# Kernel tuning notes

Hardware: AMD Instinct MI355X
Metric: run time of the kernel (lower is better)

## Reference

```python
import jax, jax.numpy as jnp
import numpy as np

EPS = 1e-12  # F.normalize eps


def quat2matrix(J):
    # J: [B, N, D, 4] in (x, y, z, w) order; normalized then reordered to (w, x, y, z)
    norm = jnp.sqrt(jnp.sum(J * J, axis=-1, keepdims=True))
    Jn = J / jnp.maximum(norm, EPS)
    x, y, z, w = Jn[..., 0], Jn[..., 1], Jn[..., 2], Jn[..., 3]
    # pytorch3d quaternion_to_matrix with q = (r, i, j, k) = (w, x, y, z)
    two_s = 2.0 / (w * w + x * x + y * y + z * z)
    r00 = 1.0 - two_s * (y * y + z * z)
    r01 = two_s * (x * y - z * w)
    r02 = two_s * (x * z + y * w)
    r10 = two_s * (x * y + z * w)
    r11 = 1.0 - two_s * (x * x + z * z)
    r12 = two_s * (y * z - x * w)
    r20 = two_s * (x * z - y * w)
    r21 = two_s * (y * z + x * w)
    r22 = 1.0 - two_s * (x * x + y * y)
    R = jnp.stack([
        jnp.stack([r00, r01, r02], axis=-1),
        jnp.stack([r10, r11, r12], axis=-1),
        jnp.stack([r20, r21, r22], axis=-1),
    ], axis=-2)  # [B, N, D, 3, 3]
    return R


def setup_inputs() -> dict:
    key = jax.random.key(0)
    k1, k2, k3, k4, k5 = jax.random.split(key, 5)
    Bb, N, D, F = 8, 4096, 256, 256  # batch, points, in_channels, out_channels
    return {
        "X": jax.random.normal(k1, (Bb, N, D, 3), dtype=jnp.float32),
        "J": jax.random.normal(k2, (Bb, N, D, 4), dtype=jnp.float32),
        "A": jax.random.normal(k3, (F, D), dtype=jnp.float32),
        "B": jax.random.normal(k4, (F, D), dtype=jnp.float32),
        "C": jax.random.normal(k5, (F, D), dtype=jnp.float32),
    }


def reference(X, J, A, B, C):
    R = quat2matrix(J)  # [B, N, D, 3, 3]
    # RTX[..., i] = (R^T X)_i = sum_k R[..., k, i] * X[..., k]
    RTX = jnp.einsum('bndki,bndk->bndi', R, X)  # [B, N, D, 3]
    rt0 = RTX[..., 0:1]
    rt1 = RTX[..., 1:2]
    rt2 = RTX[..., 2:3]
    # get_rrtx(i, R, s) = R[..., :, i] * s (column i of R scaled by scalar)
    a_term = R[..., :, 0] * rt0 + R[..., :, 1] * rt1  # [B, N, D, 3]
    b_term = R[..., :, 1] * rt0 - R[..., :, 0] * rt1
    c_term = R[..., :, 2] * rt2
    Y = (jnp.einsum('fe,bnei->bnfi', A, a_term)
         + jnp.einsum('fe,bnei->bnfi', B, b_term)
         + jnp.einsum('fe,bnei->bnfi', C, c_term))  # [B, N, F, 3]
    return Y
```

## Files before the change

kernel.cpp:

```cpp
#include <hip/hip_runtime.h>


typedef __bf16 bf16_t;
typedef __attribute__((ext_vector_type(8))) __bf16 bf16x8;
typedef __attribute__((ext_vector_type(4))) __bf16 bf16x4;
typedef __attribute__((ext_vector_type(4))) float f32x4;

constexpr int Dd  = 256;
constexpr int Gp  = 16;
constexpr int TPB = 512;

__device__ __forceinline__ bf16_t to_bf16(float f) {
    unsigned u = __builtin_bit_cast(unsigned, f);
    u += 0x7FFFu + ((u >> 16) & 1u);
    unsigned short h = (unsigned short)(u >> 16);
    return __builtin_bit_cast(bf16_t, h);
}

__device__ __forceinline__ int swz(int row, int k) {
    return row * 768 + (k ^ ((row & 7) << 3));
}

__global__ __launch_bounds__(256)
void convert_w_kernel(const float* __restrict__ A, const float* __restrict__ B,
                      const float* __restrict__ C, bf16_t* __restrict__ W)
{
    const int e4 = (blockIdx.x * 256 + threadIdx.x) * 4;
    const float* src;
    if (e4 < 65536)        src = A + e4;
    else if (e4 < 131072)  src = B + (e4 - 65536);
    else                   src = C + (e4 - 131072);
    const float4 v = *reinterpret_cast<const float4*>(src);
    bf16x4 o;
    o[0] = to_bf16(v.x); o[1] = to_bf16(v.y); o[2] = to_bf16(v.z); o[3] = to_bf16(v.w);
    *reinterpret_cast<bf16x4*>(W + e4) = o;
}

__global__ __launch_bounds__(TPB, 4)
void alaq_mfma_kernel(const float* __restrict__ X, const float* __restrict__ J,
                      const bf16_t* __restrict__ W, float* __restrict__ Y)
{
    __shared__ bf16_t TT[48 * 768];

    const int tid = threadIdx.x;
    const long bn0 = (long)blockIdx.x * Gp;
    const long ebase = bn0 * Dd;

    float4 qv[8];
    float  xv[8][3];
    #pragma unroll
    for (int rr = 0; rr < 8; ++rr) {
        const long base = ebase + rr * TPB + tid;
        qv[rr] = *reinterpret_cast<const float4*>(J + base * 4);
        const float* xp = X + base * 3;
        xv[rr][0] = xp[0]; xv[rr][1] = xp[1]; xv[rr][2] = xp[2];
    }

    #pragma unroll
    for (int rr = 0; rr < 8; ++rr) {
        const int idx = rr * TPB + tid;
        const int p = idx >> 8;
        const int e = idx & 255;

        const float4 q = qv[rr];
        const float x0 = xv[rr][0], x1 = xv[rr][1], x2 = xv[rr][2];

        const float nsq = q.x*q.x + q.y*q.y + q.z*q.z + q.w*q.w;
        const float inv = 1.0f / fmaxf(sqrtf(nsq), 1e-12f);
        const float qx = q.x*inv, qy = q.y*inv, qz = q.z*inv, qw = q.w*inv;
        const float s = 2.0f / (qw*qw + qx*qx + qy*qy + qz*qz);

        const float r00 = 1.0f - s*(qy*qy + qz*qz);
        const float r01 = s*(qx*qy - qz*qw);
        const float r02 = s*(qx*qz + qy*qw);
        const float r10 = s*(qx*qy + qz*qw);
        const float r11 = 1.0f - s*(qx*qx + qz*qz);
        const float r12 = s*(qy*qz - qx*qw);
        const float r20 = s*(qx*qz - qy*qw);
        const float r21 = s*(qy*qz + qx*qw);
        const float r22 = 1.0f - s*(qx*qx + qy*qy);

        const float rt0 = r00*x0 + r10*x1 + r20*x2;
        const float rt1 = r01*x0 + r11*x1 + r21*x2;
        const float rt2 = r02*x0 + r12*x1 + r22*x2;

        const int row = p * 3;
        TT[swz(row    ,       e)] = to_bf16(r00*rt0 + r01*rt1);
        TT[swz(row + 1,       e)] = to_bf16(r10*rt0 + r11*rt1);
        TT[swz(row + 2,       e)] = to_bf16(r20*rt0 + r21*rt1);
        TT[swz(row    , 256 + e)] = to_bf16(r01*rt0 - r00*rt1);
        TT[swz(row + 1, 256 + e)] = to_bf16(r11*rt0 - r10*rt1);
        TT[swz(row + 2, 256 + e)] = to_bf16(r21*rt0 - r20*rt1);
        TT[swz(row    , 512 + e)] = to_bf16(r02*rt2);
        TT[swz(row + 1, 512 + e)] = to_bf16(r12*rt2);
        TT[swz(row + 2, 512 + e)] = to_bf16(r22*rt2);
    }
    __syncthreads();

    const int w  = tid >> 6;
    const int l  = tid & 63;
    const int lr = l & 15;
    const int lq = l >> 4;

    f32x4 acc[3][2] = {};

    const int f0 = (2 * w) * 16 + lr;
    const bf16_t* Wf0 = W + f0 * 256 + (lq << 3);
    const bf16_t* Wf1 = Wf0 + 16 * 256;
    const int swzmask = (lr & 7) << 3;

    #pragma unroll
    for (int k0 = 0; k0 < 24; ++k0) {
        const int term = k0 >> 3;
        const int eb   = (k0 & 7) << 5;
        const bf16x8 b0 = *reinterpret_cast<const bf16x8*>(Wf0 + (term << 16) + eb);
        const bf16x8 b1 = *reinterpret_cast<const bf16x8*>(Wf1 + (term << 16) + eb);

        const int kswz = (((k0 << 5) + (lq << 3)) ^ swzmask);
        const bf16x8 a0 = *reinterpret_cast<const bf16x8*>(&TT[         lr  * 768 + kswz]);
        const bf16x8 a1 = *reinterpret_cast<const bf16x8*>(&TT[(16 +    lr) * 768 + kswz]);
        const bf16x8 a2 = *reinterpret_cast<const bf16x8*>(&TT[(32 +    lr) * 768 + kswz]);

        acc[0][0] = __builtin_amdgcn_mfma_f32_16x16x32_bf16(a0, b0, acc[0][0], 0, 0, 0);
        acc[1][0] = __builtin_amdgcn_mfma_f32_16x16x32_bf16(a1, b0, acc[1][0], 0, 0, 0);
        acc[2][0] = __builtin_amdgcn_mfma_f32_16x16x32_bf16(a2, b0, acc[2][0], 0, 0, 0);
        acc[0][1] = __builtin_amdgcn_mfma_f32_16x16x32_bf16(a0, b1, acc[0][1], 0, 0, 0);
        acc[1][1] = __builtin_amdgcn_mfma_f32_16x16x32_bf16(a1, b1, acc[1][1], 0, 0, 0);
        acc[2][1] = __builtin_amdgcn_mfma_f32_16x16x32_bf16(a2, b1, acc[2][1], 0, 0, 0);
    }

    #pragma unroll
    for (int mi = 0; mi < 3; ++mi) {
        #pragma unroll
        for (int ni = 0; ni < 2; ++ni) {
            const int f = (2 * w + ni) * 16 + lr;
            #pragma unroll
            for (int r = 0; r < 4; ++r) {
                const int m = mi * 16 + lq * 4 + r;
                const int p = m / 3;
                const int i = m - p * 3;
                Y[(bn0 + p) * 768 + f * 3 + i] = acc[mi][ni][r];
            }
        }
    }
}

extern "C" void kernel_launch(void* const* d_in, const int* in_sizes, int n_in,
                              void* d_out, int out_size, void* d_ws, size_t ws_size,
                              hipStream_t stream) {
    const float* X  = (const float*)d_in[0];
    const float* J  = (const float*)d_in[1];
    const float* A  = (const float*)d_in[2];
    const float* B  = (const float*)d_in[3];
    const float* Cm = (const float*)d_in[4];
    float* Y = (float*)d_out;
    bf16_t* W = (bf16_t*)d_ws;

    convert_w_kernel<<<192, 256, 0, stream>>>(A, B, Cm, W);

    const int nbn = in_sizes[1] / (Dd * 4);
    const int blocks = nbn / Gp;
    alaq_mfma_kernel<<<blocks, TPB, 0, stream>>>(X, J, W, Y);
}
```

Baseline: 144.5 us.

## Warp-specialize into producer/consumer waves with double-buffered LDS over chunks

Splits each 512-thread block into four producer waves that compute the rotated terms into a double-buffered LDS tile and four consumer waves that run the MFMA GEMM on the previous chunk. Each block now loops over 8 chunks of 16 points, so there are 8x fewer blocks. Each consumer wave covers 64 output channels instead of 32. The aim is to overlap the ALU-heavy quaternion work and global loads with the matrix cores. In exchange it doubles LDS per block, lowers occupancy (launch bounds 2), and uses only half the waves for each phase.

```diff
diff --git a/kernel.cpp b/kernel.cpp
--- a/kernel.cpp
+++ b/kernel.cpp
@@ -8,6 +8,7 @@
 
 constexpr int Dd  = 256;
 constexpr int Gp  = 16;
+constexpr int NCH = 8;
 constexpr int TPB = 512;
 
 __device__ __forceinline__ bf16_t to_bf16(float f) {
@@ -36,112 +37,137 @@
     *reinterpret_cast<bf16x4*>(W + e4) = o;
 }
 
-__global__ __launch_bounds__(TPB, 4)
-void alaq_mfma_kernel(const float* __restrict__ X, const float* __restrict__ J,
-                      const bf16_t* __restrict__ W, float* __restrict__ Y)
+__global__ __launch_bounds__(TPB, 2)
+void alaq_pc_kernel(const float* __restrict__ X, const float* __restrict__ J,
+                    const bf16_t* __restrict__ W, float* __restrict__ Y)
 {
-    __shared__ bf16_t TT[48 * 768];
+    __shared__ bf16_t TT[2][48 * 768];
 
     const int tid = threadIdx.x;
-    const long bn0 = (long)blockIdx.x * Gp;
-    const long ebase = bn0 * Dd;
+    const int w   = tid >> 6;
+    const int l   = tid & 63;
+    const long pair0 = (long)blockIdx.x * (Gp * NCH);
 
-    float4 qv[8];
-    float  xv[8][3];
-    #pragma unroll
-    for (int rr = 0; rr < 8; ++rr) {
-        const long base = ebase + rr * TPB + tid;
-        qv[rr] = *reinterpret_cast<const float4*>(J + base * 4);
-        const float* xp = X + base * 3;
-        xv[rr][0] = xp[0]; xv[rr][1] = xp[1]; xv[rr][2] = xp[2];
-    }
+    auto PRODUCE = [&](int chunk) {
+        bf16_t* tt = TT[chunk & 1];
+        const long eb = (pair0 + (long)chunk * Gp) * Dd;
+        #pragma unroll
+        for (int g = 0; g < 2; ++g) {
+            float4 qv[8];
+            float  xv[8][3];
+            #pragma unroll
+            for (int j = 0; j < 8; ++j) {
+                const long base = eb + (g * 8 + j) * 256 + tid;
+                qv[j] = *reinterpret_cast<const float4*>(J + base * 4);
+                const float* xp = X + base * 3;
+                xv[j][0] = xp[0]; xv[j][1] = xp[1]; xv[j][2] = xp[2];
+            }
+            #pragma unroll
+            for (int j = 0; j < 8; ++j) {
+                const int p = g * 8 + j;
+                const int e = tid;
+                const float4 q = qv[j];
+                const float x0 = xv[j][0], x1 = xv[j][1], x2 = xv[j][2];
 
-    #pragma unroll
-    for (int rr = 0; rr < 8; ++rr) {
-        const int idx = rr * TPB + tid;
-        const int p = idx >> 8;
-        const int e = idx & 255;
+                const float nsq = q.x*q.x + q.y*q.y + q.z*q.z + q.w*q.w;
+                const float inv = 1.0f / fmaxf(sqrtf(nsq), 1e-12f);
+                const float qx = q.x*inv, qy = q.y*inv, qz = q.z*inv, qw = q.w*inv;
+                const float s = 2.0f / (qw*qw + qx*qx + qy*qy + qz*qz);
 
-        const float4 q = qv[rr];
-        const float x0 = xv[rr][0], x1 = xv[rr][1], x2 = xv[rr][2];
+                const float r00 = 1.0f - s*(qy*qy + qz*qz);
+                const float r01 = s*(qx*qy - qz*qw);
+                const float r02 = s*(qx*qz + qy*qw);
+                const float r10 = s*(qx*qy + qz*qw);
+                const float r11 = 1.0f - s*(qx*qx + qz*qz);
+                const float r12 = s*(qy*qz - qx*qw);
+                const float r20 = s*(qx*qz - qy*qw);
+                const float r21 = s*(qy*qz + qx*qw);
+                const float r22 = 1.0f - s*(qx*qx + qy*qy);
 
-        const float nsq = q.x*q.x + q.y*q.y + q.z*q.z + q.w*q.w;
-        const float inv = 1.0f / fmaxf(sqrtf(nsq), 1e-12f);
-        const float qx = q.x*inv, qy = q.y*inv, qz = q.z*inv, qw = q.w*inv;
-        const float s = 2.0f / (qw*qw + qx*qx + qy*qy + qz*qz);
+                const float rt0 = r00*x0 + r10*x1 + r20*x2;
+                const float rt1 = r01*x0 + r11*x1 + r21*x2;
+                const float rt2 = r02*x0 + r12*x1 + r22*x2;
 
-        const float r00 = 1.0f - s*(qy*qy + qz*qz);
-        const float r01 = s*(qx*qy - qz*qw);
-        const float r02 = s*(qx*qz + qy*qw);
-        const float r10 = s*(qx*qy + qz*qw);
-        const float r11 = 1.0f - s*(qx*qx + qz*qz);
-        const float r12 = s*(qy*qz - qx*qw);
-        const float r20 = s*(qx*qz - qy*qw);
-        const float r21 = s*(qy*qz + qx*qw);
-        const float r22 = 1.0f - s*(qx*qx + qy*qy);
+                const int row = p * 3;
+                tt[swz(row    ,       e)] = to_bf16(r00*rt0 + r01*rt1);
+                tt[swz(row + 1,       e)] = to_bf16(r10*rt0 + r11*rt1);
+                tt[swz(row + 2,       e)] = to_bf16(r20*rt0 + r21*rt1);
+                tt[swz(row    , 256 + e)] = to_bf16(r01*rt0 - r00*rt1);
+                tt[swz(row + 1, 256 + e)] = to_bf16(r11*rt0 - r10*rt1);
+                tt[swz(row + 2, 256 + e)] = to_bf16(r21*rt0 - r20*rt1);
+                tt[swz(row    , 512 + e)] = to_bf16(r02*rt2);
+                tt[swz(row + 1, 512 + e)] = to_bf16(r12*rt2);
+                tt[swz(row + 2, 512 + e)] = to_bf16(r22*rt2);
+            }
+        }
+    };
 
-        const float rt0 = r00*x0 + r10*x1 + r20*x2;
-        const float rt1 = r01*x0 + r11*x1 + r21*x2;
-        const float rt2 = r02*x0 + r12*x1 + r22*x2;
-
-        const int row = p * 3;
-        TT[swz(row    ,       e)] = to_bf16(r00*rt0 + r01*rt1);
-        TT[swz(row + 1,       e)] = to_bf16(r10*rt0 + r11*rt1);
-        TT[swz(row + 2,       e)] = to_bf16(r20*rt0 + r21*rt1);
-        TT[swz(row    , 256 + e)] = to_bf16(r01*rt0 - r00*rt1);
-        TT[swz(row + 1, 256 + e)] = to_bf16(r11*rt0 - r10*rt1);
-        TT[swz(row + 2, 256 + e)] = to_bf16(r21*rt0 - r20*rt1);
-        TT[swz(row    , 512 + e)] = to_bf16(r02*rt2);
-        TT[swz(row + 1, 512 + e)] = to_bf16(r12*rt2);
-        TT[swz(row + 2, 512 + e)] = to_bf16(r22*rt2);
-    }
-    __syncthreads();
-
-    const int w  = tid >> 6;
-    const int l  = tid & 63;
+    const int wc = (w >= 4) ? (w - 4) : 0;
     const int lr = l & 15;
     const int lq = l >> 4;
-
-    f32x4 acc[3][2] = {};
-
-    const int f0 = (2 * w) * 16 + lr;
-    const bf16_t* Wf0 = W + f0 * 256 + (lq << 3);
-    const bf16_t* Wf1 = Wf0 + 16 * 256;
+    const bf16_t* Wb = W + ((4 * wc) * 16 + lr) * 256 + (lq << 3);
     const int swzmask = (lr & 7) << 3;
 
-    #pragma unroll
-    for (int k0 = 0; k0 < 24; ++k0) {
-        const int term = k0 >> 3;
-        const int eb   = (k0 & 7) << 5;
-        const bf16x8 b0 = *reinterpret_cast<const bf16x8*>(Wf0 + (term << 16) + eb);
-        const bf16x8 b1 = *reinterpret_cast<const bf16x8*>(Wf1 + (term << 16) + eb);
+    auto CONSUME = [&](int chunk) {
+        const bf16_t* tt = TT[chunk & 1];
+        f32x4 acc[3][4] = {};
 
-        const int kswz = (((k0 << 5) + (lq << 3)) ^ swzmask);
-        const bf16x8 a0 = *reinterpret_cast<const bf16x8*>(&TT[         lr  * 768 + kswz]);
-        const bf16x8 a1 = *reinterpret_cast<const bf16x8*>(&TT[(16 +    lr) * 768 + kswz]);
-        const bf16x8 a2 = *reinterpret_cast<const bf16x8*>(&TT[(32 +    lr) * 768 + kswz]);
+        #pragma unroll
+        for (int k0 = 0; k0 < 24; ++k0) {
+            const int term = k0 >> 3;
+            const int ebo  = (k0 & 7) << 5;
+            const bf16x8 b0 = *reinterpret_cast<const bf16x8*>(Wb                + (term << 16) + ebo);
+            const bf16x8 b1 = *reinterpret_cast<const bf16x8*>(Wb + 1 * 16 * 256 + (term << 16) + ebo);
+            const bf16x8 b2 = *reinterpret_cast<const bf16x8*>(Wb + 2 * 16 * 256 + (term << 16) + ebo);
+            const bf16x8 b3 = *reinterpret_cast<const bf16x8*>(Wb + 3 * 16 * 256 + (term << 16) + ebo);
 
-        acc[0][0] = __builtin_amdgcn_mfma_f32_16x16x32_bf16(a0, b0, acc[0][0], 0, 0, 0);
-        acc[1][0] = __builtin_amdgcn_mfma_f32_16x16x32_bf16(a1, b0, acc[1][0], 0, 0, 0);
-        acc[2][0] = __builtin_amdgcn_mfma_f32_16x16x32_bf16(a2, b0, acc[2][0], 0, 0, 0);
-        acc[0][1] = __builtin_amdgcn_mfma_f32_16x16x32_bf16(a0, b1, acc[0][1], 0, 0, 0);
-        acc[1][1] = __builtin_amdgcn_mfma_f32_16x16x32_bf16(a1, b1, acc[1][1], 0, 0, 0);
-        acc[2][1] = __builtin_amdgcn_mfma_f32_16x16x32_bf16(a2, b1, acc[2][1], 0, 0, 0);
-    }
+            const int kswz = (((k0 << 5) + (lq << 3)) ^ swzmask);
+            const bf16x8 a0 = *reinterpret_cast<const bf16x8*>(&tt[      lr  * 768 + kswz]);
+            const bf16x8 a1 = *reinterpret_cast<const bf16x8*>(&tt[(16 + lr) * 768 + kswz]);
+            const bf16x8 a2 = *reinterpret_cast<const bf16x8*>(&tt[(32 + lr) * 768 + kswz]);
 
-    #pragma unroll
-    for (int mi = 0; mi < 3; ++mi) {
+            acc[0][0] = __builtin_amdgcn_mfma_f32_16x16x32_bf16(a0, b0, acc[0][0], 0, 0, 0);
+            acc[1][0] = __builtin_amdgcn_mfma_f32_16x16x32_bf16(a1, b0, acc[1][0], 0, 0, 0);
+            acc[2][0] = __builtin_amdgcn_mfma_f32_16x16x32_bf16(a2, b0, acc[2][0], 0, 0, 0);
+            acc[0][1] = __builtin_amdgcn_mfma_f32_16x16x32_bf16(a0, b1, acc[0][1], 0, 0, 0);
+            acc[1][1] = __builtin_amdgcn_mfma_f32_16x16x32_bf16(a1, b1, acc[1][1], 0, 0, 0);
+            acc[2][1] = __builtin_amdgcn_mfma_f32_16x16x32_bf16(a2, b1, acc[2][1], 0, 0, 0);
+            acc[0][2] = __builtin_amdgcn_mfma_f32_16x16x32_bf16(a0, b2, acc[0][2], 0, 0, 0);
+            acc[1][2] = __builtin_amdgcn_mfma_f32_16x16x32_bf16(a1, b2, acc[1][2], 0, 0, 0);
+            acc[2][2] = __builtin_amdgcn_mfma_f32_16x16x32_bf16(a2, b2, acc[2][2], 0, 0, 0);
+            acc[0][3] = __builtin_amdgcn_mfma_f32_16x16x32_bf16(a0, b3, acc[0][3], 0, 0, 0);
+            acc[1][3] = __builtin_amdgcn_mfma_f32_16x16x32_bf16(a1, b3, acc[1][3], 0, 0, 0);
+            acc[2][3] = __builtin_amdgcn_mfma_f32_16x16x32_bf16(a2, b3, acc[2][3], 0, 0, 0);
+        }
+
+        float* yb = Y + (pair0 + (long)chunk * Gp) * 768;
         #pragma unroll
-        for (int ni = 0; ni < 2; ++ni) {
-            const int f = (2 * w + ni) * 16 + lr;
+        for (int mi = 0; mi < 3; ++mi) {
             #pragma unroll
             for (int r = 0; r < 4; ++r) {
                 const int m = mi * 16 + lq * 4 + r;
                 const int p = m / 3;
                 const int i = m - p * 3;
-                Y[(bn0 + p) * 768 + f * 3 + i] = acc[mi][ni][r];
+                const int rowoff = p * 768 + i;
+                #pragma unroll
+                for (int ni = 0; ni < 4; ++ni) {
+                    const int f = (4 * wc + ni) * 16 + lr;
+                    yb[rowoff + f * 3] = acc[mi][ni][r];
+                }
             }
         }
+    };
+
+    if (w < 4) PRODUCE(0);
+    __syncthreads();
+
+    for (int t = 0; t < NCH; ++t) {
+        if (w < 4) {
+            if (t + 1 < NCH) PRODUCE(t + 1);
+        } else {
+            CONSUME(t);
+        }
+        __syncthreads();
     }
 }
 
@@ -159,6 +185,6 @@
     convert_w_kernel<<<192, 256, 0, stream>>>(A, B, Cm, W);
 
     const int nbn = in_sizes[1] / (Dd * 4);
-    const int blocks = nbn / Gp;
-    alaq_mfma_kernel<<<blocks, TPB, 0, stream>>>(X, J, W, Y);
+    const int blocks = nbn / (Gp * NCH);
+    alaq_pc_kernel<<<blocks, TPB, 0, stream>>>(X, J, W, Y);
 }
```

After: 322.5 us. 123% more time.

## Make blocks persistent over chunks with async LDS prefetch of quaternions

Applied to the files above, without the earlier changes.

Each block now loops over 8 chunks of 16 points and uses 1024 threads, with one 16-wide output tile per wave instead of two. Quaternion data for the next chunk is copied straight into shared memory with global_load_lds while the MFMA loop runs on the current chunk. The aim is to overlap global loads with compute and cut the block count. In exchange it adds a 64KB LDS buffer, which lowers occupancy, and the full-block barriers around each chunk serialize the compute-transform and MFMA phases.

```diff
diff --git a/kernel.cpp b/kernel.cpp
--- a/kernel.cpp
+++ b/kernel.cpp
@@ -8,7 +8,8 @@
 
 constexpr int Dd  = 256;
 constexpr int Gp  = 16;
-constexpr int TPB = 512;
+constexpr int NCH = 8;
+constexpr int TPB = 1024;
 
 __device__ __forceinline__ bf16_t to_bf16(float f) {
     unsigned u = __builtin_bit_cast(unsigned, f);
@@ -37,111 +38,118 @@
 }
 
 __global__ __launch_bounds__(TPB, 4)
-void alaq_mfma_kernel(const float* __restrict__ X, const float* __restrict__ J,
-                      const bf16_t* __restrict__ W, float* __restrict__ Y)
+void alaq_v10_kernel(const float* __restrict__ X, const float* __restrict__ J,
+                     const bf16_t* __restrict__ W, float* __restrict__ Y)
 {
+    __shared__ float  SJ[Gp * Dd * 4];
     __shared__ bf16_t TT[48 * 768];
 
     const int tid = threadIdx.x;
-    const long bn0 = (long)blockIdx.x * Gp;
-    const long ebase = bn0 * Dd;
+    const int w   = tid >> 6;
+    const int l   = tid & 63;
+    const int lr  = l & 15;
+    const int lq  = l >> 4;
+    const long pair0 = (long)blockIdx.x * (Gp * NCH);
 
-    float4 qv[8];
-    float  xv[8][3];
-    #pragma unroll
-    for (int rr = 0; rr < 8; ++rr) {
-        const long base = ebase + rr * TPB + tid;
-        qv[rr] = *reinterpret_cast<const float4*>(J + base * 4);
-        const float* xp = X + base * 3;
-        xv[rr][0] = xp[0]; xv[rr][1] = xp[1]; xv[rr][2] = xp[2];
-    }
+    auto DMA_J = [&](int t) {
+        const char* jsrc = (const char*)J + (pair0 + (long)t * Gp) * Dd * 16;
+        char* sdst = (char*)SJ;
+        #pragma unroll
+        for (int i = 0; i < 4; ++i) {
+            const int winst = w * 4 + i;
+            __builtin_amdgcn_global_load_lds(
+                (const __attribute__((address_space(1))) void*)(jsrc + winst * 1024 + l * 16),
+                (__attribute__((address_space(3))) void*)(sdst + winst * 1024),
+                16, 0, 0);
+        }
+    };
 
-    #pragma unroll
-    for (int rr = 0; rr < 8; ++rr) {
-        const int idx = rr * TPB + tid;
-        const int p = idx >> 8;
-        const int e = idx & 255;
+    const bf16_t* Wf = W + (w * 16 + lr) * 256 + (lq << 3);
+    const int swzmask = (lr & 7) << 3;
 
-        const float4 q = qv[rr];
-        const float x0 = xv[rr][0], x1 = xv[rr][1], x2 = xv[rr][2];
-
-        const float nsq = q.x*q.x + q.y*q.y + q.z*q.z + q.w*q.w;
-        const float inv = 1.0f / fmaxf(sqrtf(nsq), 1e-12f);
-        const float qx = q.x*inv, qy = q.y*inv, qz = q.z*inv, qw = q.w*inv;
-        const float s = 2.0f / (qw*qw + qx*qx + qy*qy + qz*qz);
-
-        const float r00 = 1.0f - s*(qy*qy + qz*qz);
-        const float r01 = s*(qx*qy - qz*qw);
-        const float r02 = s*(qx*qz + qy*qw);
-        const float r10 = s*(qx*qy + qz*qw);
-        const float r11 = 1.0f - s*(qx*qx + qz*qz);
-        const float r12 = s*(qy*qz - qx*qw);
-        const float r20 = s*(qx*qz - qy*qw);
-        const float r21 = s*(qy*qz + qx*qw);
-        const float r22 = 1.0f - s*(qx*qx + qy*qy);
-
-        const float rt0 = r00*x0 + r10*x1 + r20*x2;
-        const float rt1 = r01*x0 + r11*x1 + r21*x2;
-        const float rt2 = r02*x0 + r12*x1 + r22*x2;
-
-        const int row = p * 3;
-        TT[swz(row    ,       e)] = to_bf16(r00*rt0 + r01*rt1);
-        TT[swz(row + 1,       e)] = to_bf16(r10*rt0 + r11*rt1);
-        TT[swz(row + 2,       e)] = to_bf16(r20*rt0 + r21*rt1);
-        TT[swz(row    , 256 + e)] = to_bf16(r01*rt0 - r00*rt1);
-        TT[swz(row + 1, 256 + e)] = to_bf16(r11*rt0 - r10*rt1);
-        TT[swz(row + 2, 256 + e)] = to_bf16(r21*rt0 - r20*rt1);
-        TT[swz(row    , 512 + e)] = to_bf16(r02*rt2);
-        TT[swz(row + 1, 512 + e)] = to_bf16(r12*rt2);
-        TT[swz(row + 2, 512 + e)] = to_bf16(r22*rt2);
-    }
+    DMA_J(0);
+    asm volatile("s_waitcnt vmcnt(0)" ::: "memory");
     __syncthreads();
 
-    const int w  = tid >> 6;
-    const int l  = tid & 63;
-    const int lr = l & 15;
-    const int lq = l >> 4;
+    for (int t = 0; t < NCH; ++t) {
+        const long pb = pair0 + (long)t * Gp;
 
-    f32x4 acc[3][2] = {};
+        #pragma unroll
+        for (int rr = 0; rr < 4; ++rr) {
+            const int idx = rr * TPB + tid;
+            const int p = idx >> 8;
+            const int e = idx & 255;
 
-    const int f0 = (2 * w) * 16 + lr;
-    const bf16_t* Wf0 = W + f0 * 256 + (lq << 3);
-    const bf16_t* Wf1 = Wf0 + 16 * 256;
-    const int swzmask = (lr & 7) << 3;
+            const f32x4 q = *reinterpret_cast<const f32x4*>(&SJ[idx * 4]);
+            const float* xp = X + (pb * Dd + idx) * 3;
+            const float x0 = xp[0], x1 = xp[1], x2 = xp[2];
 
-    #pragma unroll
-    for (int k0 = 0; k0 < 24; ++k0) {
-        const int term = k0 >> 3;
-        const int eb   = (k0 & 7) << 5;
-        const bf16x8 b0 = *reinterpret_cast<const bf16x8*>(Wf0 + (term << 16) + eb);
-        const bf16x8 b1 = *reinterpret_cast<const bf16x8*>(Wf1 + (term << 16) + eb);
+            const float nsq = q[0]*q[0] + q[1]*q[1] + q[2]*q[2] + q[3]*q[3];
+            const float inv = 1.0f / fmaxf(sqrtf(nsq), 1e-12f);
+            const float qx = q[0]*inv, qy = q[1]*inv, qz = q[2]*inv, qw = q[3]*inv;
+            const float s = 2.0f / (qw*qw + qx*qx + qy*qy + qz*qz);
 
-        const int kswz = (((k0 << 5) + (lq << 3)) ^ swzmask);
-        const bf16x8 a0 = *reinterpret_cast<const bf16x8*>(&TT[         lr  * 768 + kswz]);
-        const bf16x8 a1 = *reinterpret_cast<const bf16x8*>(&TT[(16 +    lr) * 768 + kswz]);
-        const bf16x8 a2 = *reinterpret_cast<const bf16x8*>(&TT[(32 +    lr) * 768 + kswz]);
+            const float r00 = 1.0f - s*(qy*qy + qz*qz);
+            const float r01 = s*(qx*qy - qz*qw);
+            const float r02 = s*(qx*qz + qy*qw);
+            const float r10 = s*(qx*qy + qz*qw);
+            const float r11 = 1.0f - s*(qx*qx + qz*qz);
+            const float r12 = s*(qy*qz - qx*qw);
+            const float r20 = s*(qx*qz - qy*qw);
+            const float r21 = s*(qy*qz + qx*qw);
+            const float r22 = 1.0f - s*(qx*qx + qy*qy);
 
-        acc[0][0] = __builtin_amdgcn_mfma_f32_16x16x32_bf16(a0, b0, acc[0][0], 0, 0, 0);
-        acc[1][0] = __builtin_amdgcn_mfma_f32_16x16x32_bf16(a1, b0, acc[1][0], 0, 0, 0);
-        acc[2][0] = __builtin_amdgcn_mfma_f32_16x16x32_bf16(a2, b0, acc[2][0], 0, 0, 0);
-        acc[0][1] = __builtin_amdgcn_mfma_f32_16x16x32_bf16(a0, b1, acc[0][1], 0, 0, 0);
-        acc[1][1] = __builtin_amdgcn_mfma_f32_16x16x32_bf16(a1, b1, acc[1][1], 0, 0, 0);
-        acc[2][1] = __builtin_amdgcn_mfma_f32_16x16x32_bf16(a2, b1, acc[2][1], 0, 0, 0);
-    }
+            const float rt0 = r00*x0 + r10*x1 + r20*x2;
+            const float rt1 = r01*x0 + r11*x1 + r21*x2;
+            const float rt2 = r02*x0 + r12*x1 + r22*x2;
 
-    #pragma unroll
-    for (int mi = 0; mi < 3; ++mi) {
+            const int row = p * 3;
+            TT[swz(row    ,       e)] = to_bf16(r00*rt0 + r01*rt1);
+            TT[swz(row + 1,       e)] = to_bf16(r10*rt0 + r11*rt1);
+            TT[swz(row + 2,       e)] = to_bf16(r20*rt0 + r21*rt1);
+            TT[swz(row    , 256 + e)] = to_bf16(r01*rt0 - r00*rt1);
+            TT[swz(row + 1, 256 + e)] = to_bf16(r11*rt0 - r10*rt1);
+            TT[swz(row + 2, 256 + e)] = to_bf16(r21*rt0 - r20*rt1);
+            TT[swz(row    , 512 + e)] = to_bf16(r02*rt2);
+            TT[swz(row + 1, 512 + e)] = to_bf16(r12*rt2);
+            TT[swz(row + 2, 512 + e)] = to_bf16(r22*rt2);
+        }
+        __syncthreads();
+
+        if (t + 1 < NCH) DMA_J(t + 1);
+
+        f32x4 acc[3] = {};
+
         #pragma unroll
-        for (int ni = 0; ni < 2; ++ni) {
-            const int f = (2 * w + ni) * 16 + lr;
+        for (int k0 = 0; k0 < 24; ++k0) {
+            const int term = k0 >> 3;
+            const int ebo  = (k0 & 7) << 5;
+            const bf16x8 b = *reinterpret_cast<const bf16x8*>(Wf + (term << 16) + ebo);
+
+            const int kswz = (((k0 << 5) + (lq << 3)) ^ swzmask);
+            const bf16x8 a0 = *reinterpret_cast<const bf16x8*>(&TT[      lr  * 768 + kswz]);
+            const bf16x8 a1 = *reinterpret_cast<const bf16x8*>(&TT[(16 + lr) * 768 + kswz]);
+            const bf16x8 a2 = *reinterpret_cast<const bf16x8*>(&TT[(32 + lr) * 768 + kswz]);
+
+            acc[0] = __builtin_amdgcn_mfma_f32_16x16x32_bf16(a0, b, acc[0], 0, 0, 0);
+            acc[1] = __builtin_amdgcn_mfma_f32_16x16x32_bf16(a1, b, acc[1], 0, 0, 0);
+            acc[2] = __builtin_amdgcn_mfma_f32_16x16x32_bf16(a2, b, acc[2], 0, 0, 0);
+        }
+
+        const int f = w * 16 + lr;
+        #pragma unroll
+        for (int mi = 0; mi < 3; ++mi) {
             #pragma unroll
             for (int r = 0; r < 4; ++r) {
                 const int m = mi * 16 + lq * 4 + r;
                 const int p = m / 3;
                 const int i = m - p * 3;
-                Y[(bn0 + p) * 768 + f * 3 + i] = acc[mi][ni][r];
+                Y[(pb + p) * 768 + f * 3 + i] = acc[mi][r];
             }
         }
+
+        asm volatile("s_waitcnt vmcnt(0)" ::: "memory");
+        __syncthreads();
     }
 }
 
@@ -159,6 +167,6 @@
     convert_w_kernel<<<192, 256, 0, stream>>>(A, B, Cm, W);
 
     const int nbn = in_sizes[1] / (Dd * 4);
-    const int blocks = nbn / Gp;
-    alaq_mfma_kernel<<<blocks, TPB, 0, stream>>>(X, J, W, Y);
+    const int blocks = nbn / (Gp * NCH);
+    alaq_v10_kernel<<<blocks, TPB, 0, stream>>>(X, J, W, Y);
 }
```

Result: slower. 292.2 us (+102.2%).

## Split fused kernel into separate terms and GEMM kernels via workspace buffer

Applied to the files above, without the earlier changes.

Unfuses the rotation-term computation from the MFMA GEMM. A grid-stride terms kernel writes bf16 terms to a global workspace buffer, and a separate GEMM kernel reads its A operands directly from global memory instead of swizzled LDS. The goal is to decouple the memory-bound elementwise phase from the MFMA phase, freeing LDS and raising occupancy. In exchange, the terms make an extra global write and read round trip of roughly 150 MB each way. A fused fallback remains for when the workspace is too small.

```diff
diff --git a/kernel.cpp b/kernel.cpp
--- a/kernel.cpp
+++ b/kernel.cpp
@@ -36,34 +36,18 @@
     *reinterpret_cast<bf16x4*>(W + e4) = o;
 }
 
-__global__ __launch_bounds__(TPB, 4)
-void alaq_mfma_kernel(const float* __restrict__ X, const float* __restrict__ J,
-                      const bf16_t* __restrict__ W, float* __restrict__ Y)
-{
-    __shared__ bf16_t TT[48 * 768];
-
-    const int tid = threadIdx.x;
-    const long bn0 = (long)blockIdx.x * Gp;
-    const long ebase = bn0 * Dd;
-
-    float4 qv[8];
-    float  xv[8][3];
-    #pragma unroll
-    for (int rr = 0; rr < 8; ++rr) {
-        const long base = ebase + rr * TPB + tid;
-        qv[rr] = *reinterpret_cast<const float4*>(J + base * 4);
-        const float* xp = X + base * 3;
-        xv[rr][0] = xp[0]; xv[rr][1] = xp[1]; xv[rr][2] = xp[2];
-    }
-
-    #pragma unroll
-    for (int rr = 0; rr < 8; ++rr) {
-        const int idx = rr * TPB + tid;
+__global__ __launch_bounds__(256)
+void terms_kernel(const float* __restrict__ X, const float* __restrict__ J,
+                  bf16_t* __restrict__ T, int nelem)
+{
+    for (int idx = blockIdx.x * 256 + threadIdx.x; idx < nelem;
+         idx += gridDim.x * 256) {
         const int p = idx >> 8;
         const int e = idx & 255;
 
-        const float4 q = qv[rr];
-        const float x0 = xv[rr][0], x1 = xv[rr][1], x2 = xv[rr][2];
+        const float4 q = *reinterpret_cast<const float4*>(J + (long)idx * 4);
+        const float* xp = X + (long)idx * 3;
+        const float x0 = xp[0], x1 = xp[1], x2 = xp[2];
 
         const float nsq = q.x*q.x + q.y*q.y + q.z*q.z + q.w*q.w;
         const float inv = 1.0f / fmaxf(sqrtf(nsq), 1e-12f);
@@ -84,18 +68,25 @@
         const float rt1 = r01*x0 + r11*x1 + r21*x2;
         const float rt2 = r02*x0 + r12*x1 + r22*x2;
 
-        const int row = p * 3;
-        TT[swz(row    ,       e)] = to_bf16(r00*rt0 + r01*rt1);
-        TT[swz(row + 1,       e)] = to_bf16(r10*rt0 + r11*rt1);
-        TT[swz(row + 2,       e)] = to_bf16(r20*rt0 + r21*rt1);
-        TT[swz(row    , 256 + e)] = to_bf16(r01*rt0 - r00*rt1);
-        TT[swz(row + 1, 256 + e)] = to_bf16(r11*rt0 - r10*rt1);
-        TT[swz(row + 2, 256 + e)] = to_bf16(r21*rt0 - r20*rt1);
-        TT[swz(row    , 512 + e)] = to_bf16(r02*rt2);
-        TT[swz(row + 1, 512 + e)] = to_bf16(r12*rt2);
-        TT[swz(row + 2, 512 + e)] = to_bf16(r22*rt2);
-    }
-    __syncthreads();
+        bf16_t* t = T + (long)(p * 3) * 768 + e;
+        t[0]              = to_bf16(r00*rt0 + r01*rt1);
+        t[768]            = to_bf16(r10*rt0 + r11*rt1);
+        t[1536]           = to_bf16(r20*rt0 + r21*rt1);
+        t[256]            = to_bf16(r01*rt0 - r00*rt1);
+        t[768 + 256]      = to_bf16(r11*rt0 - r10*rt1);
+        t[1536 + 256]     = to_bf16(r21*rt0 - r20*rt1);
+        t[512]            = to_bf16(r02*rt2);
+        t[768 + 512]      = to_bf16(r12*rt2);
+        t[1536 + 512]     = to_bf16(r22*rt2);
+    }
+}
+
+__global__ __launch_bounds__(TPB)
+void gemm_kernel(const bf16_t* __restrict__ T, const bf16_t* __restrict__ W,
+                 float* __restrict__ Y)
+{
+    const int tid = threadIdx.x;
+    const long bn0 = (long)blockIdx.x * Gp;
 
     const int w  = tid >> 6;
     const int l  = tid & 63;
@@ -104,10 +95,9 @@
 
     f32x4 acc[3][2] = {};
 
-    const int f0 = (2 * w) * 16 + lr;
-    const bf16_t* Wf0 = W + f0 * 256 + (lq << 3);
+    const bf16_t* Wf0 = W + ((2 * w) * 16 + lr) * 256 + (lq << 3);
     const bf16_t* Wf1 = Wf0 + 16 * 256;
-    const int swzmask = (lr & 7) << 3;
+    const bf16_t* Ta = T + (bn0 * 3 + lr) * 768 + (lq << 3);
 
     #pragma unroll
     for (int k0 = 0; k0 < 24; ++k0) {
@@ -116,10 +106,10 @@
         const bf16x8 b0 = *reinterpret_cast<const bf16x8*>(Wf0 + (term << 16) + eb);
         const bf16x8 b1 = *reinterpret_cast<const bf16x8*>(Wf1 + (term << 16) + eb);
 
-        const int kswz = (((k0 << 5) + (lq << 3)) ^ swzmask);
-        const bf16x8 a0 = *reinterpret_cast<const bf16x8*>(&TT[         lr  * 768 + kswz]);
-        const bf16x8 a1 = *reinterpret_cast<const bf16x8*>(&TT[(16 +    lr) * 768 + kswz]);
-        const bf16x8 a2 = *reinterpret_cast<const bf16x8*>(&TT[(32 +    lr) * 768 + kswz]);
+        const int kof = k0 << 5;
+        const bf16x8 a0 = *reinterpret_cast<const bf16x8*>(Ta              + kof);
+        const bf16x8 a1 = *reinterpret_cast<const bf16x8*>(Ta + 16 * 768   + kof);
+        const bf16x8 a2 = *reinterpret_cast<const bf16x8*>(Ta + 32 * 768   + kof);
 
         acc[0][0] = __builtin_amdgcn_mfma_f32_16x16x32_bf16(a0, b0, acc[0][0], 0, 0, 0);
         acc[1][0] = __builtin_amdgcn_mfma_f32_16x16x32_bf16(a1, b0, acc[1][0], 0, 0, 0);
@@ -145,6 +135,96 @@
     }
 }
 
+__global__ __launch_bounds__(TPB, 4)
+void alaq_fused_v3(const float* __restrict__ X, const float* __restrict__ J,
+                   const bf16_t* __restrict__ W, float* __restrict__ Y)
+{
+    __shared__ bf16_t TT[48 * 768];
+    const int tid = threadIdx.x;
+    const long bn0 = (long)blockIdx.x * Gp;
+    const long ebase = bn0 * Dd;
+
+    #pragma unroll
+    for (int rr = 0; rr < 8; ++rr) {
+        const int idx = rr * TPB + tid;
+        const int p = idx >> 8;
+        const int e = idx & 255;
+        const long base = ebase + idx;
+        const float4 q = *reinterpret_cast<const float4*>(J + base * 4);
+        const float* xp = X + base * 3;
+        const float x0 = xp[0], x1 = xp[1], x2 = xp[2];
+        const float nsq = q.x*q.x + q.y*q.y + q.z*q.z + q.w*q.w;
+        const float inv = 1.0f / fmaxf(sqrtf(nsq), 1e-12f);
+        const float qx = q.x*inv, qy = q.y*inv, qz = q.z*inv, qw = q.w*inv;
+        const float s = 2.0f / (qw*qw + qx*qx + qy*qy + qz*qz);
+        const float r00 = 1.0f - s*(qy*qy + qz*qz);
+        const float r01 = s*(qx*qy - qz*qw);
+        const float r02 = s*(qx*qz + qy*qw);
+        const float r10 = s*(qx*qy + qz*qw);
+        const float r11 = 1.0f - s*(qx*qx + qz*qz);
+        const float r12 = s*(qy*qz - qx*qw);
+        const float r20 = s*(qx*qz - qy*qw);
+        const float r21 = s*(qy*qz + qx*qw);
+        const float r22 = 1.0f - s*(qx*qx + qy*qy);
+        const float rt0 = r00*x0 + r10*x1 + r20*x2;
+        const float rt1 = r01*x0 + r11*x1 + r21*x2;
+        const float rt2 = r02*x0 + r12*x1 + r22*x2;
+        const int row = p * 3;
+        TT[swz(row    ,       e)] = to_bf16(r00*rt0 + r01*rt1);
+        TT[swz(row + 1,       e)] = to_bf16(r10*rt0 + r11*rt1);
+        TT[swz(row + 2,       e)] = to_bf16(r20*rt0 + r21*rt1);
+        TT[swz(row    , 256 + e)] = to_bf16(r01*rt0 - r00*rt1);
+        TT[swz(row + 1, 256 + e)] = to_bf16(r11*rt0 - r10*rt1);
+        TT[swz(row + 2, 256 + e)] = to_bf16(r21*rt0 - r20*rt1);
+        TT[swz(row    , 512 + e)] = to_bf16(r02*rt2);
+        TT[swz(row + 1, 512 + e)] = to_bf16(r12*rt2);
+        TT[swz(row + 2, 512 + e)] = to_bf16(r22*rt2);
+    }
+    __syncthreads();
+
+    const int w  = tid >> 6;
+    const int l  = tid & 63;
+    const int lr = l & 15;
+    const int lq = l >> 4;
+    f32x4 acc[3][2] = {};
+    const bf16_t* Wf0 = W + ((2 * w) * 16 + lr) * 256 + (lq << 3);
+    const bf16_t* Wf1 = Wf0 + 16 * 256;
+    const int swzmask = (lr & 7) << 3;
+
+    #pragma unroll
+    for (int k0 = 0; k0 < 24; ++k0) {
+        const int term = k0 >> 3;
+        const int eb   = (k0 & 7) << 5;
+        const bf16x8 b0 = *reinterpret_cast<const bf16x8*>(Wf0 + (term << 16) + eb);
+        const bf16x8 b1 = *reinterpret_cast<const bf16x8*>(Wf1 + (term << 16) + eb);
+        const int kswz = (((k0 << 5) + (lq << 3)) ^ swzmask);
+        const bf16x8 a0 = *reinterpret_cast<const bf16x8*>(&TT[      lr  * 768 + kswz]);
+        const bf16x8 a1 = *reinterpret_cast<const bf16x8*>(&TT[(16 + lr) * 768 + kswz]);
+        const bf16x8 a2 = *reinterpret_cast<const bf16x8*>(&TT[(32 + lr) * 768 + kswz]);
+        acc[0][0] = __builtin_amdgcn_mfma_f32_16x16x32_bf16(a0, b0, acc[0][0], 0, 0, 0);
+        acc[1][0] = __builtin_amdgcn_mfma_f32_16x16x32_bf16(a1, b0, acc[1][0], 0, 0, 0);
+        acc[2][0] = __builtin_amdgcn_mfma_f32_16x16x32_bf16(a2, b0, acc[2][0], 0, 0, 0);
+        acc[0][1] = __builtin_amdgcn_mfma_f32_16x16x32_bf16(a0, b1, acc[0][1], 0, 0, 0);
+        acc[1][1] = __builtin_amdgcn_mfma_f32_16x16x32_bf16(a1, b1, acc[1][1], 0, 0, 0);
+        acc[2][1] = __builtin_amdgcn_mfma_f32_16x16x32_bf16(a2, b1, acc[2][1], 0, 0, 0);
+    }
+
+    #pragma unroll
+    for (int mi = 0; mi < 3; ++mi) {
+        #pragma unroll
+        for (int ni = 0; ni < 2; ++ni) {
+            const int f = (2 * w + ni) * 16 + lr;
+            #pragma unroll
+            for (int r = 0; r < 4; ++r) {
+                const int m = mi * 16 + lq * 4 + r;
+                const int p = m / 3;
+                const int i = m - p * 3;
+                Y[(bn0 + p) * 768 + f * 3 + i] = acc[mi][ni][r];
+            }
+        }
+    }
+}
+
 extern "C" void kernel_launch(void* const* d_in, const int* in_sizes, int n_in,
                               void* d_out, int out_size, void* d_ws, size_t ws_size,
                               hipStream_t stream) {
@@ -154,11 +234,20 @@
     const float* B  = (const float*)d_in[3];
     const float* Cm = (const float*)d_in[4];
     float* Y = (float*)d_out;
+
     bf16_t* W = (bf16_t*)d_ws;
+    const int nbn = in_sizes[1] / (Dd * 4);
+    const int nelem = nbn * Dd;
+    const size_t t_bytes = (size_t)nbn * 3 * 768 * sizeof(bf16_t);
+    const size_t need = 393216 + t_bytes;
 
     convert_w_kernel<<<192, 256, 0, stream>>>(A, B, Cm, W);
 
-    const int nbn = in_sizes[1] / (Dd * 4);
-    const int blocks = nbn / Gp;
-    alaq_mfma_kernel<<<blocks, TPB, 0, stream>>>(X, J, W, Y);
-}
+    if (ws_size >= need) {
+        bf16_t* T = (bf16_t*)((char*)d_ws + 393216);
+        terms_kernel<<<2048, 256, 0, stream>>>(X, J, T, nelem);
+        gemm_kernel<<<nbn / Gp, TPB, 0, stream>>>(T, W, Y);
+    } else {
+        alaq_fused_v3<<<nbn / Gp, TPB, 0, stream>>>(X, J, W, Y);
+    }
+}
```

Result: slower. 313.7 us (+117.1%).
